# Kernel tuning notes

Measured on AMD Instinct MI355X. Metric: run time of the kernel, lower is better.

## Reference

```python
import jax, jax.numpy as jnp
from jax import lax
import numpy as np

NT, NB, NF = 4000, 128, 40
NPOS = 500
SHARP = 1.0


def setup_inputs() -> dict:
    key = jax.random.key(0)
    k1, k2, k3, k4 = jax.random.split(key, 4)
    x = jax.random.normal(k1, (NT, NB, NF), dtype=jnp.float32)
    move_idx = jax.random.randint(k2, (NB, NPOS - 1), 0, NF)
    stay_idx = jax.random.randint(k3, (NB, NPOS), 0, NF)
    seqlens = jax.random.randint(k4, (NB,), 1, NPOS + 1)  # in [1, NPOS]
    return {"x": x, "move_idx": move_idx, "stay_idx": stay_idx, "seqlens": seqlens}


def reference(x, move_idx, stay_idx, seqlens):
    # x: [nt, nb, 40]; move_idx: [nb, npos-1]; stay_idx: [nb, npos]; seqlens: [nb]
    nt, nb, nf = x.shape
    npos = stay_idx.shape[1]
    fwd0 = jnp.full((nb, npos), -1e30, dtype=x.dtype).at[:, 0].set(0.0)

    def step(prev, xt):
        xts = xt * SHARP                                        # [nb, nf]
        stay = jnp.take_along_axis(xts, stay_idx, axis=1) + prev            # [nb, npos]
        move = jnp.take_along_axis(xts, move_idx, axis=1) + prev[:, :-1]    # [nb, npos-1]
        new = stay.at[:, 1:].set(jnp.logaddexp(move, stay[:, 1:]))
        return new, None

    fwd, _ = lax.scan(step, fwd0, x)
    # gather score at final sequence position, normalize
    out = -jnp.take_along_axis(fwd, (seqlens - 1)[:, None], axis=1) / (SHARP * nt)
    return out  # [nb, 1]
```

## Files before the change

### kernel.cpp

```cpp
#include <hip/hip_runtime.h>


typedef float f32x4 __attribute__((ext_vector_type(4)));

constexpr int NT   = 4000;
constexpr int NB   = 128;
constexpr int NF   = 40;
constexpr int NPOS = 500;
constexpr int NWIN = NT / 4;
constexpr float C_SCALE   = 1.4426950408889634f;
constexpr float OUT_SCALE = -0.6931471805599453f / 4000.f;
constexpr float NEGF = -1e30f;

__device__ __forceinline__ float dpp_shr1(float v) {
    int r = __builtin_amdgcn_update_dpp(
        __float_as_int(NEGF), __float_as_int(v),
        0x138 , 0xF, 0xF, false);
    return __int_as_float(r);
}

__device__ __forceinline__ float lae2(float A, float B) {
    float mx = fmaxf(A, B);
    float d  = A - B;
    return mx + __log2f(1.0f + exp2f(-fabsf(d)));
}

__global__ void __launch_bounds__(256, 1) flipflop_fwd(
    const float* __restrict__ x,
    const int*   __restrict__ move_idx,
    const int*   __restrict__ stay_idx,
    const int*   __restrict__ seqlens,
    float*       __restrict__ out)
{
    const int b    = blockIdx.x;
    const int tid  = threadIdx.x;
    const int lane = tid & 63;
    const int wv   = tid >> 6;

    __shared__ f32x4 xring[8][NF];
    __shared__ float ex[2][3][4];

    const int pbase = 124 * wv + 2 * lane;
    const int p0 = pbase, p1 = pbase + 1;

    const int sidx0 = stay_idx[b * NPOS + p0];
    const int sidx1 = stay_idx[b * NPOS + p1];
    const int midx0 = move_idx[b * (NPOS - 1) + ((p0 >= 1) ? p0 - 1 : 0)];
    const int midx1 = move_idx[b * (NPOS - 1) + p0];

    float F0 = (p0 == 0) ? 0.0f : NEGF;
    float F1 = NEGF;

    unsigned ring_u = (unsigned)(unsigned long long)
        (__attribute__((address_space(3))) char*)&xring[0][0];
    const unsigned a_s0 = ring_u + (unsigned)sidx0 * 16u;
    const unsigned a_m0 = ring_u + (unsigned)midx0 * 16u;
    const unsigned a_s1 = ring_u + (unsigned)sidx1 * 16u;
    const unsigned a_m1 = ring_u + (unsigned)midx1 * 16u;

    f32x4 gbuf[2][4];

#define GATHER(SLOT, G) do {                                                        \
    asm volatile("ds_read_b128 %0, %1 offset:%c2"                                   \
                 : "=v"(gbuf[G][0]) : "v"(a_s0), "i"((SLOT) * 640));                \
    asm volatile("ds_read_b128 %0, %1 offset:%c2"                                   \
                 : "=v"(gbuf[G][1]) : "v"(a_m0), "i"((SLOT) * 640));                \
    asm volatile("ds_read_b128 %0, %1 offset:%c2"                                   \
                 : "=v"(gbuf[G][2]) : "v"(a_s1), "i"((SLOT) * 640));                \
    asm volatile("ds_read_b128 %0, %1 offset:%c2"                                   \
                 : "=v"(gbuf[G][3]) : "v"(a_m1), "i"((SLOT) * 640));                \
} while (0)

#define COMPUTE(G) do {                                                             \
    _Pragma("unroll")                                                               \
    for (int i = 0; i < 4; ++i) {                                                   \
        float nb = dpp_shr1(F1);                                                    \
        float a0 = fmaf(gbuf[G][1][i], C_SCALE, nb);                                \
        float b0 = fmaf(gbuf[G][0][i], C_SCALE, F0);                                \
        float a1 = fmaf(gbuf[G][3][i], C_SCALE, F0);                                \
        float b1 = fmaf(gbuf[G][2][i], C_SCALE, F1);                                \
        F0 = lae2(a0, b0);                                                          \
        F1 = lae2(a1, b1);                                                          \
    }                                                                               \
} while (0)

    const int tt = lane & 3;
    const float* gk0 = x + (size_t)b * NF + (lane >> 2);

    auto stagewin = [&](int w) {
        const int slot = w & 7;
        int t = w * 4 + tt;
        if (t > NT - 1) t = NT - 1;
        const size_t toff = (size_t)t * (NB * NF);
        auto dst = (__attribute__((address_space(3))) char*)&xring[slot][0];
        __builtin_amdgcn_global_load_lds(
            (const __attribute__((address_space(1))) void*)(gk0 + toff),
            (__attribute__((address_space(3))) void*)(dst), 4, 0, 0);
        __builtin_amdgcn_global_load_lds(
            (const __attribute__((address_space(1))) void*)(gk0 + 16 + toff),
            (__attribute__((address_space(3))) void*)(dst + 256), 4, 0, 0);
        if (lane < 32)
            __builtin_amdgcn_global_load_lds(
                (const __attribute__((address_space(1))) void*)(gk0 + 32 + toff),
                (__attribute__((address_space(3))) void*)(dst + 512), 4, 0, 0);
    };

    if (wv == 0) {
        for (int s = 0; s < 7; ++s) stagewin(s);
    }
    asm volatile("s_waitcnt vmcnt(15)" ::: "memory");
    asm volatile("s_waitcnt lgkmcnt(0)" ::: "memory");
    __builtin_amdgcn_sched_barrier(0);
    __builtin_amdgcn_s_barrier();
    asm volatile("" ::: "memory");

    GATHER(0, 0);

#define BODY(W) do {                                                               \
    const int w_ = wbase + (W);                                                     \
    if (wv == 0) stagewin(w_ + 7);                           \
    GATHER(((W) + 1) & 7, ((W) + 1) & 1);                     \
    COMPUTE((W) & 1);                                                               \
    if (wv < 3 && lane >= 62) {                                                     \
        ex[(W) & 1][wv][(lane - 62) * 2 + 0] = F0;                                  \
        ex[(W) & 1][wv][(lane - 62) * 2 + 1] = F1;                                  \
    }                                                                               \
    asm volatile("s_waitcnt vmcnt(15)" ::: "memory");          \
    asm volatile("s_waitcnt lgkmcnt(0)" ::: "memory");         \
    __builtin_amdgcn_sched_barrier(0);                                              \
    __builtin_amdgcn_s_barrier();                                                   \
    asm volatile("" ::: "memory");                                                  \
    if (wv >= 1 && lane < 2) {                                                      \
        F0 = ex[(W) & 1][wv - 1][lane * 2 + 0];                                     \
        F1 = ex[(W) & 1][wv - 1][lane * 2 + 1];                                     \
    }                                                                               \
} while (0)

    for (int wbase = 0; wbase < NWIN; wbase += 8) {
        BODY(0); BODY(1); BODY(2); BODY(3);
        BODY(4); BODY(5); BODY(6); BODY(7);
    }

#undef BODY
#undef COMPUTE
#undef GATHER

    const int pf  = seqlens[b] - 1;
    const bool own = (wv == 0) || (lane >= 2);
    if (own) {
        if (p0 == pf)      out[b] = F0 * OUT_SCALE;
        else if (p1 == pf) out[b] = F1 * OUT_SCALE;
    }
}

extern "C" void kernel_launch(void* const* d_in, const int* in_sizes, int n_in,
                              void* d_out, int out_size, void* d_ws, size_t ws_size,
                              hipStream_t stream) {
    const float* x        = (const float*)d_in[0];
    const int*   move_idx = (const int*)d_in[1];
    const int*   stay_idx = (const int*)d_in[2];
    const int*   seqlens  = (const int*)d_in[3];
    float*       out      = (float*)d_out;

    flipflop_fwd<<<dim3(NB), dim3(256), 0, stream>>>(x, move_idx, stay_idx, seqlens, out);
}
```

Before: 373.4 us.

## Process two batch rows per block with interleaved independent recurrences

Each 256-thread block now runs the forward recurrence for two batch elements at once. It keeps two sets of state registers, two LDS rings and two index sets, and interleaves the two dependency chains inside the compute loop for instruction-level parallelism. Staging for the second batch moves to wave 1, so the per-window barriers and boundary exchanges are shared across both rows. The launch grid is halved. The aim is to hide the serial exp/log latency and to amortise barrier cost, at the price of fewer active CUs and higher register pressure.

```diff
diff --git a/kernel.cpp b/kernel.cpp
--- a/kernel.cpp
+++ b/kernel.cpp
@@ -32,82 +32,100 @@
     const int*   __restrict__ seqlens,
     float*       __restrict__ out)
 {
-    const int b    = blockIdx.x;
+    const int bA   = blockIdx.x * 2;
+    const int bB   = bA + 1;
     const int tid  = threadIdx.x;
     const int lane = tid & 63;
     const int wv   = tid >> 6;
 
-    __shared__ f32x4 xring[8][NF];
-    __shared__ float ex[2][3][4];
+    __shared__ f32x4 xring[2][8][NF];
+    __shared__ float ex[2][3][2][4];
 
     const int pbase = 124 * wv + 2 * lane;
     const int p0 = pbase, p1 = pbase + 1;
 
-    const int sidx0 = stay_idx[b * NPOS + p0];
-    const int sidx1 = stay_idx[b * NPOS + p1];
-    const int midx0 = move_idx[b * (NPOS - 1) + ((p0 >= 1) ? p0 - 1 : 0)];
-    const int midx1 = move_idx[b * (NPOS - 1) + p0];
+    const int sA0 = stay_idx[bA * NPOS + p0];
+    const int sA1 = stay_idx[bA * NPOS + p1];
+    const int mA0 = move_idx[bA * (NPOS - 1) + ((p0 >= 1) ? p0 - 1 : 0)];
+    const int mA1 = move_idx[bA * (NPOS - 1) + p0];
+    const int sB0 = stay_idx[bB * NPOS + p0];
+    const int sB1 = stay_idx[bB * NPOS + p1];
+    const int mB0 = move_idx[bB * (NPOS - 1) + ((p0 >= 1) ? p0 - 1 : 0)];
+    const int mB1 = move_idx[bB * (NPOS - 1) + p0];
 
-    float F0 = (p0 == 0) ? 0.0f : NEGF;
-    float F1 = NEGF;
+    float FA0 = (p0 == 0) ? 0.0f : NEGF, FA1 = NEGF;
+    float FB0 = FA0,                     FB1 = NEGF;
 
-    unsigned ring_u = (unsigned)(unsigned long long)
-        (__attribute__((address_space(3))) char*)&xring[0][0];
-    const unsigned a_s0 = ring_u + (unsigned)sidx0 * 16u;
-    const unsigned a_m0 = ring_u + (unsigned)midx0 * 16u;
-    const unsigned a_s1 = ring_u + (unsigned)sidx1 * 16u;
-    const unsigned a_m1 = ring_u + (unsigned)midx1 * 16u;
+    unsigned ringA = (unsigned)(unsigned long long)
+        (__attribute__((address_space(3))) char*)&xring[0][0][0];
+    unsigned ringB = (unsigned)(unsigned long long)
+        (__attribute__((address_space(3))) char*)&xring[1][0][0];
+    const unsigned aA_s0 = ringA + (unsigned)sA0 * 16u;
+    const unsigned aA_m0 = ringA + (unsigned)mA0 * 16u;
+    const unsigned aA_s1 = ringA + (unsigned)sA1 * 16u;
+    const unsigned aA_m1 = ringA + (unsigned)mA1 * 16u;
+    const unsigned aB_s0 = ringB + (unsigned)sB0 * 16u;
+    const unsigned aB_m0 = ringB + (unsigned)mB0 * 16u;
+    const unsigned aB_s1 = ringB + (unsigned)sB1 * 16u;
+    const unsigned aB_m1 = ringB + (unsigned)mB1 * 16u;
 
-    f32x4 gbuf[2][4];
+    f32x4 g[2][8];
 
-#define GATHER(SLOT, G) do {                                                        \
-    asm volatile("ds_read_b128 %0, %1 offset:%c2"                                   \
-                 : "=v"(gbuf[G][0]) : "v"(a_s0), "i"((SLOT) * 640));                \
-    asm volatile("ds_read_b128 %0, %1 offset:%c2"                                   \
-                 : "=v"(gbuf[G][1]) : "v"(a_m0), "i"((SLOT) * 640));                \
-    asm volatile("ds_read_b128 %0, %1 offset:%c2"                                   \
-                 : "=v"(gbuf[G][2]) : "v"(a_s1), "i"((SLOT) * 640));                \
-    asm volatile("ds_read_b128 %0, %1 offset:%c2"                                   \
-                 : "=v"(gbuf[G][3]) : "v"(a_m1), "i"((SLOT) * 640));                \
+#define DSR(DST, ADDR, SLOT)                                                    \
+    asm volatile("ds_read_b128 %0, %1 offset:%c2"                               \
+                 : "=v"(DST) : "v"(ADDR), "i"((SLOT) * 640))
+
+#define GATHER(SLOT, G) do {                                                    \
+    DSR(g[G][0], aA_s0, SLOT); DSR(g[G][1], aA_m0, SLOT);                       \
+    DSR(g[G][2], aA_s1, SLOT); DSR(g[G][3], aA_m1, SLOT);                       \
+    DSR(g[G][4], aB_s0, SLOT); DSR(g[G][5], aB_m0, SLOT);                       \
+    DSR(g[G][6], aB_s1, SLOT); DSR(g[G][7], aB_m1, SLOT);                       \
 } while (0)
 
-#define COMPUTE(G) do {                                                             \
-    _Pragma("unroll")                                                               \
-    for (int i = 0; i < 4; ++i) {                                                   \
-        float nb = dpp_shr1(F1);                                                    \
-        float a0 = fmaf(gbuf[G][1][i], C_SCALE, nb);                                \
-        float b0 = fmaf(gbuf[G][0][i], C_SCALE, F0);                                \
-        float a1 = fmaf(gbuf[G][3][i], C_SCALE, F0);                                \
-        float b1 = fmaf(gbuf[G][2][i], C_SCALE, F1);                                \
-        F0 = lae2(a0, b0);                                                          \
-        F1 = lae2(a1, b1);                                                          \
-    }                                                                               \
+#define COMPUTE(G) do {                                                         \
+    _Pragma("unroll")                                                           \
+    for (int i = 0; i < 4; ++i) {                                               \
+        float nbA = dpp_shr1(FA1);                                              \
+        float nbB = dpp_shr1(FB1);                                              \
+        float xaA0 = fmaf(g[G][1][i], C_SCALE, nbA);                            \
+        float xbA0 = fmaf(g[G][0][i], C_SCALE, FA0);                            \
+        float xaA1 = fmaf(g[G][3][i], C_SCALE, FA0);                            \
+        float xbA1 = fmaf(g[G][2][i], C_SCALE, FA1);                            \
+        float xaB0 = fmaf(g[G][5][i], C_SCALE, nbB);                            \
+        float xbB0 = fmaf(g[G][4][i], C_SCALE, FB0);                            \
+        float xaB1 = fmaf(g[G][7][i], C_SCALE, FB0);                            \
+        float xbB1 = fmaf(g[G][6][i], C_SCALE, FB1);                            \
+        FA0 = lae2(xaA0, xbA0);                                                 \
+        FB0 = lae2(xaB0, xbB0);                                                 \
+        FA1 = lae2(xaA1, xbA1);                                                 \
+        FB1 = lae2(xaB1, xbB1);                                                 \
+    }                                                                           \
 } while (0)
 
     const int tt = lane & 3;
-    const float* gk0 = x + (size_t)b * NF + (lane >> 2);
+    const float* gkA = x + (size_t)bA * NF + (lane >> 2);
+    const float* gkB = x + (size_t)bB * NF + (lane >> 2);
 
-    auto stagewin = [&](int w) {
+    auto stagewin = [&](int w, const float* gk, int batch) {
         const int slot = w & 7;
         int t = w * 4 + tt;
         if (t > NT - 1) t = NT - 1;
         const size_t toff = (size_t)t * (NB * NF);
-        auto dst = (__attribute__((address_space(3))) char*)&xring[slot][0];
+        auto dst = (__attribute__((address_space(3))) char*)&xring[batch][slot][0];
         __builtin_amdgcn_global_load_lds(
-            (const __attribute__((address_space(1))) void*)(gk0 + toff),
+            (const __attribute__((address_space(1))) void*)(gk + toff),
             (__attribute__((address_space(3))) void*)(dst), 4, 0, 0);
         __builtin_amdgcn_global_load_lds(
-            (const __attribute__((address_space(1))) void*)(gk0 + 16 + toff),
+            (const __attribute__((address_space(1))) void*)(gk + 16 + toff),
             (__attribute__((address_space(3))) void*)(dst + 256), 4, 0, 0);
         if (lane < 32)
             __builtin_amdgcn_global_load_lds(
-                (const __attribute__((address_space(1))) void*)(gk0 + 32 + toff),
+                (const __attribute__((address_space(1))) void*)(gk + 32 + toff),
                 (__attribute__((address_space(3))) void*)(dst + 512), 4, 0, 0);
     };
 
-    if (wv == 0) {
-        for (int s = 0; s < 7; ++s) stagewin(s);
-    }
+    if (wv == 0)      { for (int s = 0; s < 7; ++s) stagewin(s, gkA, 0); }
+    else if (wv == 1) { for (int s = 0; s < 7; ++s) stagewin(s, gkB, 1); }
     asm volatile("s_waitcnt vmcnt(15)" ::: "memory");
     asm volatile("s_waitcnt lgkmcnt(0)" ::: "memory");
     __builtin_amdgcn_sched_barrier(0);
@@ -116,24 +134,28 @@
 
     GATHER(0, 0);
 
-#define BODY(W) do {                                                               \
-    const int w_ = wbase + (W);                                                     \
-    if (wv == 0) stagewin(w_ + 7);                           \
-    GATHER(((W) + 1) & 7, ((W) + 1) & 1);                     \
-    COMPUTE((W) & 1);                                                               \
-    if (wv < 3 && lane >= 62) {                                                     \
-        ex[(W) & 1][wv][(lane - 62) * 2 + 0] = F0;                                  \
-        ex[(W) & 1][wv][(lane - 62) * 2 + 1] = F1;                                  \
-    }                                                                               \
-    asm volatile("s_waitcnt vmcnt(15)" ::: "memory");          \
-    asm volatile("s_waitcnt lgkmcnt(0)" ::: "memory");         \
-    __builtin_amdgcn_sched_barrier(0);                                              \
-    __builtin_amdgcn_s_barrier();                                                   \
-    asm volatile("" ::: "memory");                                                  \
-    if (wv >= 1 && lane < 2) {                                                      \
-        F0 = ex[(W) & 1][wv - 1][lane * 2 + 0];                                     \
-        F1 = ex[(W) & 1][wv - 1][lane * 2 + 1];                                     \
-    }                                                                               \
+#define BODY(W) do {                                                            \
+    const int w_ = wbase + (W);                                                 \
+    if (wv == 0)      stagewin(w_ + 7, gkA, 0);                                 \
+    else if (wv == 1) stagewin(w_ + 7, gkB, 1);                                 \
+    GATHER(((W) + 1) & 7, ((W) + 1) & 1);                  \
+    COMPUTE((W) & 1);                                                           \
+    if (wv < 3 && lane >= 62) {                                                 \
+        const int h = (lane - 62) * 2;                                          \
+        ex[(W) & 1][wv][0][h + 0] = FA0; ex[(W) & 1][wv][0][h + 1] = FA1;       \
+        ex[(W) & 1][wv][1][h + 0] = FB0; ex[(W) & 1][wv][1][h + 1] = FB1;       \
+    }                                                                           \
+    asm volatile("s_waitcnt vmcnt(15)" ::: "memory");      \
+    asm volatile("s_waitcnt lgkmcnt(0)" ::: "memory");     \
+    __builtin_amdgcn_sched_barrier(0);                                          \
+    __builtin_amdgcn_s_barrier();                                               \
+    asm volatile("" ::: "memory");                                              \
+    if (wv >= 1 && lane < 2) {                                                  \
+        FA0 = ex[(W) & 1][wv - 1][0][lane * 2 + 0];                             \
+        FA1 = ex[(W) & 1][wv - 1][0][lane * 2 + 1];                             \
+        FB0 = ex[(W) & 1][wv - 1][1][lane * 2 + 0];                             \
+        FB1 = ex[(W) & 1][wv - 1][1][lane * 2 + 1];                             \
+    }                                                                           \
 } while (0)
 
     for (int wbase = 0; wbase < NWIN; wbase += 8) {
@@ -144,12 +166,16 @@
 #undef BODY
 #undef COMPUTE
 #undef GATHER
+#undef DSR
 
-    const int pf  = seqlens[b] - 1;
+    const int pfA = seqlens[bA] - 1;
+    const int pfB = seqlens[bB] - 1;
     const bool own = (wv == 0) || (lane >= 2);
     if (own) {
-        if (p0 == pf)      out[b] = F0 * OUT_SCALE;
-        else if (p1 == pf) out[b] = F1 * OUT_SCALE;
+        if (p0 == pfA)      out[bA] = FA0 * OUT_SCALE;
+        else if (p1 == pfA) out[bA] = FA1 * OUT_SCALE;
+        if (p0 == pfB)      out[bB] = FB0 * OUT_SCALE;
+        else if (p1 == pfB) out[bB] = FB1 * OUT_SCALE;
     }
 }
 
@@ -162,5 +188,5 @@
     const int*   seqlens  = (const int*)d_in[3];
     float*       out      = (float*)d_out;
 
-    flipflop_fwd<<<dim3(NB), dim3(256), 0, stream>>>(x, move_idx, stay_idx, seqlens, out);
+    flipflop_fwd<<<dim3(NB / 2), dim3(256), 0, stream>>>(x, move_idx, stay_idx, seqlens, out);
 }
```

Result: slower. 663.1 us (+77.6%).

## Use ghost-zone overlap to sync waves once per 40 timesteps

Applied to the files above, without the earlier changes.

Each wave now owns 125 positions plus a 40-position ghost region overlapping its left neighbour, with 4 positions per lane. The wave recomputes the halo redundantly instead of exchanging boundary values with the neighbour wave every 4 timesteps. Boundary values are exchanged and the workgroup barrier runs once per superstep of 10 windows (40 timesteps). x is staged in double-buffered halves of 10 windows rather than an 8-slot ring. This cuts barrier and synchronisation overhead, at the cost of redundant computation, more registers, and coarser prefetch. Correctness depends on the 40-step dependency cone fitting inside the ghost width.

```diff
diff --git a/kernel.cpp b/kernel.cpp
--- a/kernel.cpp
+++ b/kernel.cpp
@@ -7,7 +7,10 @@
 constexpr int NB   = 128;
 constexpr int NF   = 40;
 constexpr int NPOS = 500;
-constexpr int NWIN = NT / 4;
+constexpr int WPS  = 10;
+constexpr int NSS  = NT / (WPS*4);
+constexpr int OWN  = 125;
+constexpr int GH   = 40;
 constexpr float C_SCALE   = 1.4426950408889634f;
 constexpr float OUT_SCALE = -0.6931471805599453f / 4000.f;
 constexpr float NEGF = -1e30f;
@@ -37,119 +40,164 @@
     const int lane = tid & 63;
     const int wv   = tid >> 6;
 
-    __shared__ f32x4 xring[8][NF];
-    __shared__ float ex[2][3][4];
-
-    const int pbase = 124 * wv + 2 * lane;
-    const int p0 = pbase, p1 = pbase + 1;
-
-    const int sidx0 = stay_idx[b * NPOS + p0];
-    const int sidx1 = stay_idx[b * NPOS + p1];
-    const int midx0 = move_idx[b * (NPOS - 1) + ((p0 >= 1) ? p0 - 1 : 0)];
-    const int midx1 = move_idx[b * (NPOS - 1) + p0];
-
-    float F0 = (p0 == 0) ? 0.0f : NEGF;
-    float F1 = NEGF;
-
-    unsigned ring_u = (unsigned)(unsigned long long)
-        (__attribute__((address_space(3))) char*)&xring[0][0];
-    const unsigned a_s0 = ring_u + (unsigned)sidx0 * 16u;
-    const unsigned a_m0 = ring_u + (unsigned)midx0 * 16u;
-    const unsigned a_s1 = ring_u + (unsigned)sidx1 * 16u;
-    const unsigned a_m1 = ring_u + (unsigned)midx1 * 16u;
-
-    f32x4 gbuf[2][4];
-
-#define GATHER(SLOT, G) do {                                                        \
-    asm volatile("ds_read_b128 %0, %1 offset:%c2"                                   \
-                 : "=v"(gbuf[G][0]) : "v"(a_s0), "i"((SLOT) * 640));                \
-    asm volatile("ds_read_b128 %0, %1 offset:%c2"                                   \
-                 : "=v"(gbuf[G][1]) : "v"(a_m0), "i"((SLOT) * 640));                \
-    asm volatile("ds_read_b128 %0, %1 offset:%c2"                                   \
-                 : "=v"(gbuf[G][2]) : "v"(a_s1), "i"((SLOT) * 640));                \
-    asm volatile("ds_read_b128 %0, %1 offset:%c2"                                   \
-                 : "=v"(gbuf[G][3]) : "v"(a_m1), "i"((SLOT) * 640));                \
-} while (0)
-
-#define COMPUTE(G) do {                                                             \
-    _Pragma("unroll")                                                               \
-    for (int i = 0; i < 4; ++i) {                                                   \
-        float nb = dpp_shr1(F1);                                                    \
-        float a0 = fmaf(gbuf[G][1][i], C_SCALE, nb);                                \
-        float b0 = fmaf(gbuf[G][0][i], C_SCALE, F0);                                \
-        float a1 = fmaf(gbuf[G][3][i], C_SCALE, F0);                                \
-        float b1 = fmaf(gbuf[G][2][i], C_SCALE, F1);                                \
-        F0 = lae2(a0, b0);                                                          \
-        F1 = lae2(a1, b1);                                                          \
-    }                                                                               \
+    __shared__ f32x4 xbuf[2][WPS][NF];
+    __shared__ float exh[2][3][GH];
+
+    const int startw = (wv == 0) ? 0 : (OWN * wv - GH);
+    const int pb = startw + 4 * lane;
+
+    const int q0 = pb + 0 > 499 ? 499 : pb + 0;
+    const int q1 = pb + 1 > 499 ? 499 : pb + 1;
+    const int q2 = pb + 2 > 499 ? 499 : pb + 2;
+    const int q3 = pb + 3 > 499 ? 499 : pb + 3;
+    const int s0 = stay_idx[b * NPOS + q0];
+    const int s1 = stay_idx[b * NPOS + q1];
+    const int s2 = stay_idx[b * NPOS + q2];
+    const int s3 = stay_idx[b * NPOS + q3];
+    const int m0 = move_idx[b * (NPOS - 1) + (q0 >= 1 ? q0 - 1 : 0)];
+    const int m1 = move_idx[b * (NPOS - 1) + (q1 >= 1 ? q1 - 1 : 0)];
+    const int m2 = move_idx[b * (NPOS - 1) + (q2 >= 1 ? q2 - 1 : 0)];
+    const int m3 = move_idx[b * (NPOS - 1) + (q3 >= 1 ? q3 - 1 : 0)];
+
+    float F0 = (pb == 0) ? 0.0f : NEGF;
+    float F1 = NEGF, F2 = NEGF, F3 = NEGF;
+
+    unsigned base_u = (unsigned)(unsigned long long)
+        (__attribute__((address_space(3))) char*)&xbuf[0][0][0];
+    const unsigned aS0 = base_u + (unsigned)s0 * 16u;
+    const unsigned aM0 = base_u + (unsigned)m0 * 16u;
+    const unsigned aS1 = base_u + (unsigned)s1 * 16u;
+    const unsigned aM1 = base_u + (unsigned)m1 * 16u;
+    const unsigned aS2 = base_u + (unsigned)s2 * 16u;
+    const unsigned aM2 = base_u + (unsigned)m2 * 16u;
+    const unsigned aS3 = base_u + (unsigned)s3 * 16u;
+    const unsigned aM3 = base_u + (unsigned)m3 * 16u;
+
+    f32x4 g[2][8];
+
+#define DSR(DST, ADDR, OFS)                                                     \
+    asm volatile("ds_read_b128 %0, %1 offset:%c2"                               \
+                 : "=v"(DST) : "v"(ADDR), "i"(OFS))
+
+#define GATHER(H, WIN, G) do {                                                  \
+    DSR(g[G][0], aS0, ((H) * WPS + (WIN)) * 640);                               \
+    DSR(g[G][1], aM0, ((H) * WPS + (WIN)) * 640);                               \
+    DSR(g[G][2], aS1, ((H) * WPS + (WIN)) * 640);                               \
+    DSR(g[G][3], aM1, ((H) * WPS + (WIN)) * 640);                               \
+    DSR(g[G][4], aS2, ((H) * WPS + (WIN)) * 640);                               \
+    DSR(g[G][5], aM2, ((H) * WPS + (WIN)) * 640);                               \
+    DSR(g[G][6], aS3, ((H) * WPS + (WIN)) * 640);                               \
+    DSR(g[G][7], aM3, ((H) * WPS + (WIN)) * 640);                               \
+} while (0)
+
+#define COMPUTE(G) do {                                                         \
+    _Pragma("unroll")                                                           \
+    for (int i = 0; i < 4; ++i) {                                               \
+        float nb = dpp_shr1(F3);                                                \
+        float xa0 = fmaf(g[G][1][i], C_SCALE, nb);                              \
+        float xb0 = fmaf(g[G][0][i], C_SCALE, F0);                              \
+        float xa1 = fmaf(g[G][3][i], C_SCALE, F0);                              \
+        float xb1 = fmaf(g[G][2][i], C_SCALE, F1);                              \
+        float xa2 = fmaf(g[G][5][i], C_SCALE, F1);                              \
+        float xb2 = fmaf(g[G][4][i], C_SCALE, F2);                              \
+        float xa3 = fmaf(g[G][7][i], C_SCALE, F2);                              \
+        float xb3 = fmaf(g[G][6][i], C_SCALE, F3);                              \
+        F0 = lae2(xa0, xb0);                                                    \
+        F1 = lae2(xa1, xb1);                                                    \
+        F2 = lae2(xa2, xb2);                                                    \
+        F3 = lae2(xa3, xb3);                                                    \
+    }                                                                           \
 } while (0)
 
     const int tt = lane & 3;
     const float* gk0 = x + (size_t)b * NF + (lane >> 2);
 
-    auto stagewin = [&](int w) {
-        const int slot = w & 7;
-        int t = w * 4 + tt;
-        if (t > NT - 1) t = NT - 1;
-        const size_t toff = (size_t)t * (NB * NF);
-        auto dst = (__attribute__((address_space(3))) char*)&xring[slot][0];
-        __builtin_amdgcn_global_load_lds(
-            (const __attribute__((address_space(1))) void*)(gk0 + toff),
-            (__attribute__((address_space(3))) void*)(dst), 4, 0, 0);
-        __builtin_amdgcn_global_load_lds(
-            (const __attribute__((address_space(1))) void*)(gk0 + 16 + toff),
-            (__attribute__((address_space(3))) void*)(dst + 256), 4, 0, 0);
-        if (lane < 32)
+    auto stage_half = [&](int ss) {
+        const int h = ss & 1;
+        #pragma unroll
+        for (int win = 0; win < WPS; ++win) {
+            const int t = (ss * WPS + win) * 4 + tt;
+            const size_t toff = (size_t)t * (NB * NF);
+            auto dst = (__attribute__((address_space(3))) char*)&xbuf[h][win][0];
             __builtin_amdgcn_global_load_lds(
-                (const __attribute__((address_space(1))) void*)(gk0 + 32 + toff),
-                (__attribute__((address_space(3))) void*)(dst + 512), 4, 0, 0);
+                (const __attribute__((address_space(1))) void*)(gk0 + toff),
+                (__attribute__((address_space(3))) void*)(dst), 4, 0, 0);
+            __builtin_amdgcn_global_load_lds(
+                (const __attribute__((address_space(1))) void*)(gk0 + 16 + toff),
+                (__attribute__((address_space(3))) void*)(dst + 256), 4, 0, 0);
+            if (lane < 32)
+                __builtin_amdgcn_global_load_lds(
+                    (const __attribute__((address_space(1))) void*)(gk0 + 32 + toff),
+                    (__attribute__((address_space(3))) void*)(dst + 512), 4, 0, 0);
+        }
     };
 
+    const int rb = OWN * (wv + 1) - GH;
+
+#define PUB(FV, J, PAR) do {                                                    \
+    unsigned o_ = (unsigned)(pb + (J) - rb);                                    \
+    if (o_ < (unsigned)GH) exh[PAR][wv][o_] = (FV);                             \
+} while (0)
+
+#define WINBODY(H, W) do {                                                      \
+    GATHER(H, (W) + 1, ((W) + 1) & 1);                                          \
+    asm volatile("s_waitcnt lgkmcnt(8)" ::: "memory");                          \
+    __builtin_amdgcn_sched_barrier(0);                                          \
+    COMPUTE((W) & 1);                                                           \
+} while (0)
+
+#define SUPER(H) do {                                                           \
+    const int ss = s + (H);                                                     \
+    if (wv == 0 && ss < NSS - 1) stage_half(ss + 1);         \
+    GATHER(H, 0, 0);                                                            \
+    WINBODY(H, 0); WINBODY(H, 1); WINBODY(H, 2); WINBODY(H, 3);                 \
+    WINBODY(H, 4); WINBODY(H, 5); WINBODY(H, 6); WINBODY(H, 7);                 \
+    WINBODY(H, 8);                                                              \
+    asm volatile("s_waitcnt lgkmcnt(0)" ::: "memory");     \
+    __builtin_amdgcn_sched_barrier(0);                                          \
+    COMPUTE(1);                                             \
+    if (wv < 3) { PUB(F0, 0, H); PUB(F1, 1, H); PUB(F2, 2, H); PUB(F3, 3, H); } \
+    asm volatile("s_waitcnt vmcnt(0)" ::: "memory");       \
+    asm volatile("s_waitcnt lgkmcnt(0)" ::: "memory");     \
+    __builtin_amdgcn_sched_barrier(0);                                          \
+    __builtin_amdgcn_s_barrier();                                               \
+    asm volatile("" ::: "memory");                                              \
+    if (wv >= 1 && lane < GH / 4) {                    \
+        F0 = exh[H][wv - 1][4 * lane + 0];                                      \
+        F1 = exh[H][wv - 1][4 * lane + 1];                                      \
+        F2 = exh[H][wv - 1][4 * lane + 2];                                      \
+        F3 = exh[H][wv - 1][4 * lane + 3];                                      \
+    }                                                                           \
+} while (0)
+
     if (wv == 0) {
-        for (int s = 0; s < 7; ++s) stagewin(s);
+        stage_half(0);
+        asm volatile("s_waitcnt vmcnt(0)" ::: "memory");
     }
-    asm volatile("s_waitcnt vmcnt(15)" ::: "memory");
     asm volatile("s_waitcnt lgkmcnt(0)" ::: "memory");
     __builtin_amdgcn_sched_barrier(0);
     __builtin_amdgcn_s_barrier();
     asm volatile("" ::: "memory");
 
-    GATHER(0, 0);
-
-#define BODY(W) do {                                                               \
-    const int w_ = wbase + (W);                                                     \
-    if (wv == 0) stagewin(w_ + 7);                           \
-    GATHER(((W) + 1) & 7, ((W) + 1) & 1);                     \
-    COMPUTE((W) & 1);                                                               \
-    if (wv < 3 && lane >= 62) {                                                     \
-        ex[(W) & 1][wv][(lane - 62) * 2 + 0] = F0;                                  \
-        ex[(W) & 1][wv][(lane - 62) * 2 + 1] = F1;                                  \
-    }                                                                               \
-    asm volatile("s_waitcnt vmcnt(15)" ::: "memory");          \
-    asm volatile("s_waitcnt lgkmcnt(0)" ::: "memory");         \
-    __builtin_amdgcn_sched_barrier(0);                                              \
-    __builtin_amdgcn_s_barrier();                                                   \
-    asm volatile("" ::: "memory");                                                  \
-    if (wv >= 1 && lane < 2) {                                                      \
-        F0 = ex[(W) & 1][wv - 1][lane * 2 + 0];                                     \
-        F1 = ex[(W) & 1][wv - 1][lane * 2 + 1];                                     \
-    }                                                                               \
-} while (0)
-
-    for (int wbase = 0; wbase < NWIN; wbase += 8) {
-        BODY(0); BODY(1); BODY(2); BODY(3);
-        BODY(4); BODY(5); BODY(6); BODY(7);
+    for (int s = 0; s < NSS; s += 2) {
+        SUPER(0);
+        SUPER(1);
     }
 
-#undef BODY
+#undef SUPER
+#undef WINBODY
+#undef PUB
 #undef COMPUTE
 #undef GATHER
-
-    const int pf  = seqlens[b] - 1;
-    const bool own = (wv == 0) || (lane >= 2);
-    if (own) {
-        if (p0 == pf)      out[b] = F0 * OUT_SCALE;
-        else if (p1 == pf) out[b] = F1 * OUT_SCALE;
+#undef DSR
+
+    const int pf = seqlens[b] - 1;
+    const int lo = OWN * wv;
+    if (pf >= lo && pf < lo + OWN) {
+        if      (pf == pb + 0) out[b] = F0 * OUT_SCALE;
+        else if (pf == pb + 1) out[b] = F1 * OUT_SCALE;
+        else if (pf == pb + 2) out[b] = F2 * OUT_SCALE;
+        else if (pf == pb + 3) out[b] = F3 * OUT_SCALE;
     }
 }
 
```

Measured after the change: 524.9 us, median of 5. +40.6%, slower.
